# Optimization experiments

Measured on AMD Instinct MI355X. Metric: run time of the kernel, lower is better.

Reference implementation:

```python
import jax, jax.numpy as jnp
import numpy as np

N, E = 40000, 640000
DIN, HID, H = 512, 128, 4
C = HID  # per-head channels; H*C == 512 == DIN
BN_EPS = 1e-5


def setup_inputs() -> dict:
    key = jax.random.key(0)
    ks = jax.random.split(key, 32)
    sc = 0.05
    d = {}
    d["x"] = jax.random.normal(ks[0], (N, DIN), jnp.float32)
    d["edge_index"] = jax.random.randint(ks[1], (2, E), 0, N)
    i = 2
    for l in (1, 2, 3):
        d[f"W{l}"] = jax.random.normal(ks[i], (DIN, H * C), jnp.float32) * sc; i += 1
        d[f"as{l}"] = jax.random.normal(ks[i], (H, C), jnp.float32) * sc; i += 1
        d[f"ad{l}"] = jax.random.normal(ks[i], (H, C), jnp.float32) * sc; i += 1
        d[f"b{l}"] = jnp.zeros((H * C,), jnp.float32)
        d[f"g{l}"] = jnp.ones((H * C,), jnp.float32)
        d[f"be{l}"] = jnp.zeros((H * C,), jnp.float32)
    d["Wg1"] = jax.random.normal(ks[i], (H * C, HID), jnp.float32) * sc; i += 1
    d["bg1"] = jnp.zeros((HID,), jnp.float32)
    d["Wg2"] = jax.random.normal(ks[i], (HID, 1), jnp.float32) * sc; i += 1
    d["bg2"] = jnp.zeros((1,), jnp.float32)
    d["Wf1"] = jax.random.normal(ks[i], (H * C, HID), jnp.float32) * sc; i += 1
    d["bf1"] = jnp.zeros((HID,), jnp.float32)
    d["Wf2"] = jax.random.normal(ks[i], (HID, HID), jnp.float32) * sc; i += 1
    d["bf2"] = jnp.zeros((HID,), jnp.float32)
    d["Wp"] = jax.random.normal(ks[i], (HID + H * C, HID), jnp.float32) * sc; i += 1
    d["bp"] = jnp.zeros((HID,), jnp.float32)
    return d


def _gat(x, src, dst, W, a_s, a_d, b):
    # PyG GATConv (concat=True, negative_slope=0.2, self-loops already in src/dst)
    n = x.shape[0]
    h = (x @ W).reshape(n, H, C)                      # [N,H,C]
    es = jnp.einsum('nhc,hc->nh', h, a_s)             # alpha_src per node
    ed = jnp.einsum('nhc,hc->nh', h, a_d)             # alpha_dst per node
    e = jax.nn.leaky_relu(es[src] + ed[dst], 0.2)     # [Etot,H]
    m = jax.ops.segment_max(e, dst, num_segments=n)   # softmax over incoming edges
    ex = jnp.exp(e - m[dst])
    s = jax.ops.segment_sum(ex, dst, num_segments=n)
    w = ex / (s[dst] + 1e-16)                         # [Etot,H]
    out = jax.ops.segment_sum(w[:, :, None] * h[src], dst, num_segments=n)
    return out.reshape(n, H * C) + b


def _bn(x, g, b):
    mu = x.mean(0)
    var = x.var(0)
    return (x - mu) * jax.lax.rsqrt(var + BN_EPS) * g + b


def reference(x, edge_index,
              W1, as1, ad1, b1, g1, be1,
              W2, as2, ad2, b2, g2, be2,
              W3, as3, ad3, b3, g3, be3,
              Wg1, bg1, Wg2, bg2, Wf1, bf1, Wf2, bf2, Wp, bp):
    n = x.shape[0]
    loops = jnp.arange(n)
    src = jnp.concatenate([edge_index[0], loops])
    dst = jnp.concatenate([edge_index[1], loops])

    h = jax.nn.leaky_relu(_bn(_gat(x, src, dst, W1, as1, ad1, b1), g1, be1), 0.2)
    h_res = h
    h = jax.nn.leaky_relu(_bn(_gat(h, src, dst, W2, as2, ad2, b2), g2, be2), 0.2) + h_res
    h_res = h
    h = jax.nn.leaky_relu(_bn(_gat(h, src, dst, W3, as3, ad3, b3), g3, be3), 0.2) + h_res

    attn_scores = (jnp.tanh(h @ Wg1 + bg1) @ Wg2 + bg2)[:, 0]   # [N]
    attn_w = jax.nn.softmax(attn_scores)                        # softmax over all nodes
    feat = jax.nn.relu(h @ Wf1 + bf1) @ Wf2 + bf2               # [N,HID]
    gated = (attn_w[:, None] * feat).sum(0)                     # [HID]
    global_pooled = h.mean(0, keepdims=True)                    # batch=None -> one graph
    combined = jnp.concatenate([gated[None, :], global_pooled], axis=-1)  # [1,640]
    out = (combined @ Wp + bp)[0]                               # [HID]
    return out, attn_scores
```

## Files before the change

### kernel.cpp

```cpp
#include <hip/hip_runtime.h>
#include <math.h>

#define N_NODES 40000
#define M_PAD   40064
#define N_EDGES 640000
#define ETOT    (N_EDGES + N_NODES)
#define DINC    512
#define NHEAD   4
#define CHD     128
#define BN_EPS  1e-5f

typedef __attribute__((ext_vector_type(8))) short bf16x8;
typedef __attribute__((ext_vector_type(4))) float f32x4;

static __device__ __forceinline__ float lrelu(float x) { return x > 0.f ? x : 0.2f * x; }

static __device__ __forceinline__ unsigned short f2b(float f) {
    union { float f; unsigned int u; } v; v.f = f;
    unsigned int r = (v.u + 0x7fff + ((v.u >> 16) & 1)) >> 16;
    return (unsigned short)r;
}
static __device__ __forceinline__ float b2f(unsigned short b) {
    union { unsigned int u; float f; } v; v.u = ((unsigned int)b) << 16;
    return v.f;
}
static __device__ __forceinline__ float lo16(unsigned int u) {
    union { unsigned int u; float f; } v; v.u = u << 16; return v.f;
}
static __device__ __forceinline__ float hi16(unsigned int u) {
    union { unsigned int u; float f; } v; v.u = u & 0xffff0000u; return v.f;
}

static __device__ __forceinline__ void fma8(float* acc, uint4 hv, float wgt) {
    acc[0] += wgt * lo16(hv.x); acc[1] += wgt * hi16(hv.x);
    acc[2] += wgt * lo16(hv.y); acc[3] += wgt * hi16(hv.y);
    acc[4] += wgt * lo16(hv.z); acc[5] += wgt * hi16(hv.z);
    acc[6] += wgt * lo16(hv.w); acc[7] += wgt * hi16(hv.w);
}

#define GLDS16(g, l) __builtin_amdgcn_global_load_lds( \
    (__attribute__((address_space(1))) void*)(g),      \
    (__attribute__((address_space(3))) void*)(l), 16, 0, 0)

__global__ void k_degree(const int* __restrict__ ei, int* __restrict__ cnt) {
    int e = blockIdx.x * 256 + threadIdx.x;
    if (e < ETOT) {
        int dst = (e < N_EDGES) ? ei[N_EDGES + e] : (e - N_EDGES);
        atomicAdd(&cnt[dst], 1);
    }
}

__global__ __launch_bounds__(64) void k_scan1(const int* __restrict__ deg, int* __restrict__ bsum) {
    int lane = threadIdx.x;
    int v = deg[blockIdx.x * 64 + lane];
#pragma unroll
    for (int off = 32; off; off >>= 1) v += __shfl_xor(v, off);
    if (lane == 0) bsum[blockIdx.x] = v;
}

__global__ __launch_bounds__(1024) void k_scan2(const int* __restrict__ bsum, int* __restrict__ bpref,
                                                int* __restrict__ rowptr) {
    __shared__ int buf[1024];
    int tid = threadIdx.x;
    int v = (tid < 625) ? bsum[tid] : 0;
    buf[tid] = v;
    __syncthreads();
    for (int off = 1; off < 1024; off <<= 1) {
        int t = (tid >= off) ? buf[tid - off] : 0;
        __syncthreads();
        buf[tid] += t;
        __syncthreads();
    }
    if (tid < 625) bpref[tid] = buf[tid] - v;
    if (tid == 0) rowptr[N_NODES] = ETOT;
}

__global__ __launch_bounds__(64) void k_scan3(const int* __restrict__ deg, const int* __restrict__ bpref,
                                              int* __restrict__ rowptr) {
    int lane = threadIdx.x;
    int i = blockIdx.x * 64 + lane;
    int v = deg[i];
    int inc = v;
#pragma unroll
    for (int off = 1; off < 64; off <<= 1) {
        int t = __shfl_up(inc, off);
        if (lane >= off) inc += t;
    }
    rowptr[i] = bpref[blockIdx.x] + inc - v;
}

__global__ void k_fill(const int* __restrict__ ei, const int* __restrict__ rowptr,
                       int* __restrict__ cnt, int* __restrict__ csr_src) {
    int e = blockIdx.x * 256 + threadIdx.x;
    if (e < ETOT) {
        int src, dst;
        if (e < N_EDGES) { src = ei[e]; dst = ei[N_EDGES + e]; }
        else             { src = e - N_EDGES; dst = src; }
        int pos = rowptr[dst] + atomicAdd(&cnt[dst], 1);
        csr_src[pos] = src;
    }
}

__global__ __launch_bounds__(256) void k_cvtx(const float4* __restrict__ xin, uint4* __restrict__ xb) {
    size_t i = (size_t)blockIdx.x * 256 + threadIdx.x;
    float4 a = xin[i * 2], b = xin[i * 2 + 1];
    uint4 o;
    o.x = (unsigned)f2b(a.x) | ((unsigned)f2b(a.y) << 16);
    o.y = (unsigned)f2b(a.z) | ((unsigned)f2b(a.w) << 16);
    o.z = (unsigned)f2b(b.x) | ((unsigned)f2b(b.y) << 16);
    o.w = (unsigned)f2b(b.z) | ((unsigned)f2b(b.w) << 16);
    xb[i] = o;
}

__global__ __launch_bounds__(256) void k_cvtw(const float* __restrict__ W, unsigned short* __restrict__ Wt,
                                              int K, int Nn) {
    int idx = blockIdx.x * 256 + threadIdx.x;
    int k = idx / Nn, n = idx % Nn;
    Wt[(size_t)n * K + k] = f2b(W[idx]);
}

template<int CBF16, int EPI>
__global__ __launch_bounds__(256) void k_gemm_mfma(const unsigned short* __restrict__ A,
                                                   const unsigned short* __restrict__ Bt,
                                                   void* __restrict__ Cout,
                                                   int Nn, int K, int nbn,
                                                   const float* __restrict__ as_,
                                                   const float* __restrict__ ad_,
                                                   float* __restrict__ es,
                                                   float* __restrict__ ed) {
    __shared__ alignas(16) unsigned short As[128 * 64];
    __shared__ alignas(16) unsigned short Bs[128 * 64];
    const int tid  = threadIdx.x;
    const int wv   = tid >> 6;
    const int lane = tid & 63;
    const int bm = (blockIdx.x / nbn) * 128;
    const int bn = (blockIdx.x % nbn) * 128;
    const int wm = (wv >> 1) * 64;
    const int wn = (wv & 1) * 64;

    const int srow = lane >> 3;
    const int scol = (((lane & 7) ^ srow) * 8);
    const size_t a_base = (size_t)(bm + wv * 32 + srow) * K + scol;
    const size_t b_base = (size_t)(bn + wv * 32 + srow) * K + scol;

    f32x4 acc[4][4] = {};

    for (int k0 = 0; k0 < K; k0 += 64) {
#pragma unroll
        for (int q = 0; q < 4; ++q)
            GLDS16(A + a_base + (size_t)q * 8 * K + k0, &As[(wv * 32 + q * 8) * 64]);
#pragma unroll
        for (int q = 0; q < 4; ++q)
            GLDS16(Bt + b_base + (size_t)q * 8 * K + k0, &Bs[(wv * 32 + q * 8) * 64]);
        __syncthreads();

        const int r0 = lane & 15;
#pragma unroll
        for (int ks = 0; ks < 2; ++ks) {
            const int c = ks * 4 + (lane >> 4);
            bf16x8 af[4], bfr[4];
#pragma unroll
            for (int i = 0; i < 4; ++i) {
                int row = wm + i * 16 + r0;
                af[i] = *(const bf16x8*)&As[row * 64 + ((c ^ (row & 7)) * 8)];
            }
#pragma unroll
            for (int j = 0; j < 4; ++j) {
                int row = wn + j * 16 + r0;
                bfr[j] = *(const bf16x8*)&Bs[row * 64 + ((c ^ (row & 7)) * 8)];
            }
#pragma unroll
            for (int i = 0; i < 4; ++i)
#pragma unroll
                for (int j = 0; j < 4; ++j)
                    acc[i][j] = __builtin_amdgcn_mfma_f32_16x16x32_bf16(af[i], bfr[j], acc[i][j], 0, 0, 0);
        }
        __syncthreads();
    }

    const int crow0 = bm + wm + (lane >> 4) * 4;
    const int ccol  = bn + wn + (lane & 15);
#pragma unroll
    for (int i = 0; i < 4; ++i)
#pragma unroll
        for (int j = 0; j < 4; ++j)
#pragma unroll
            for (int r = 0; r < 4; ++r) {
                size_t off = (size_t)(crow0 + i * 16 + r) * Nn + ccol + j * 16;
                if (CBF16) ((unsigned short*)Cout)[off] = f2b(acc[i][j][r]);
                else       ((float*)Cout)[off] = acc[i][j][r];
            }

    if (EPI) {
        const int head = bn >> 7;
        float asv[4], adv[4];
#pragma unroll
        for (int j = 0; j < 4; ++j) {
            int cc = head * CHD + wn + j * 16 + (lane & 15);
            asv[j] = as_[cc];
            adv[j] = ad_[cc];
        }
        float* sE = (float*)As;
        sE[tid] = 0.f;
        __syncthreads();
#pragma unroll
        for (int i = 0; i < 4; ++i)
#pragma unroll
            for (int r = 0; r < 4; ++r) {
                float e = acc[i][0][r] * asv[0] + acc[i][1][r] * asv[1]
                        + acc[i][2][r] * asv[2] + acc[i][3][r] * asv[3];
                float d = acc[i][0][r] * adv[0] + acc[i][1][r] * adv[1]
                        + acc[i][2][r] * adv[2] + acc[i][3][r] * adv[3];
#pragma unroll
                for (int off = 8; off; off >>= 1) {
                    e += __shfl_xor(e, off);
                    d += __shfl_xor(d, off);
                }
                if ((lane & 15) == 0) {
                    int rloc = wm + i * 16 + (lane >> 4) * 4 + r;
                    atomicAdd(&sE[rloc], e);
                    atomicAdd(&sE[128 + rloc], d);
                }
            }
        __syncthreads();
        if (tid < 128) {
            es[(size_t)(bm + tid) * NHEAD + head] = sE[tid];
            ed[(size_t)(bm + tid) * NHEAD + head] = sE[128 + tid];
        }
    }
}

__global__ __launch_bounds__(256) void k_wts(const float4* __restrict__ es4,
                                             const float4* __restrict__ ed4,
                                             const int* __restrict__ rowptr,
                                             const int* __restrict__ csr_src,
                                             float4* __restrict__ wbuf4,
                                             float4* __restrict__ inv4) {
    int n = blockIdx.x * 4 + (threadIdx.x >> 6);
    int lane = threadIdx.x & 63;
    int start = rowptr[n], end = rowptr[n + 1];
    float4 edn = ed4[n];
    float4 mx = make_float4(-1e30f, -1e30f, -1e30f, -1e30f);
    for (int j0 = start; j0 < end; j0 += 64) {
        int j = j0 + lane;
        if (j < end) {
            int s = csr_src[j];
            float4 e = es4[s];
            mx.x = fmaxf(mx.x, lrelu(e.x + edn.x));
            mx.y = fmaxf(mx.y, lrelu(e.y + edn.y));
            mx.z = fmaxf(mx.z, lrelu(e.z + edn.z));
            mx.w = fmaxf(mx.w, lrelu(e.w + edn.w));
        }
    }
#pragma unroll
    for (int off = 32; off; off >>= 1) {
        mx.x = fmaxf(mx.x, __shfl_xor(mx.x, off));
        mx.y = fmaxf(mx.y, __shfl_xor(mx.y, off));
        mx.z = fmaxf(mx.z, __shfl_xor(mx.z, off));
        mx.w = fmaxf(mx.w, __shfl_xor(mx.w, off));
    }
    float4 sum = make_float4(0.f, 0.f, 0.f, 0.f);
    for (int j0 = start; j0 < end; j0 += 64) {
        int j = j0 + lane;
        if (j < end) {
            int s = csr_src[j];
            float4 e = es4[s];
            float4 ex;
            ex.x = expf(lrelu(e.x + edn.x) - mx.x);
            ex.y = expf(lrelu(e.y + edn.y) - mx.y);
            ex.z = expf(lrelu(e.z + edn.z) - mx.z);
            ex.w = expf(lrelu(e.w + edn.w) - mx.w);
            wbuf4[j] = ex;
            sum.x += ex.x; sum.y += ex.y; sum.z += ex.z; sum.w += ex.w;
        }
    }
#pragma unroll
    for (int off = 32; off; off >>= 1) {
        sum.x += __shfl_xor(sum.x, off);
        sum.y += __shfl_xor(sum.y, off);
        sum.z += __shfl_xor(sum.z, off);
        sum.w += __shfl_xor(sum.w, off);
    }
    if (lane == 0) {
        float4 iv;
        iv.x = 1.f / (sum.x + 1e-16f);
        iv.y = 1.f / (sum.y + 1e-16f);
        iv.z = 1.f / (sum.z + 1e-16f);
        iv.w = 1.f / (sum.w + 1e-16f);
        inv4[n] = iv;
    }
}

__global__ __launch_bounds__(256) void k_agg(const unsigned short* __restrict__ hb,
                                             const int* __restrict__ rowptr,
                                             const int* __restrict__ csr_src,
                                             const float* __restrict__ wbuf,
                                             const float* __restrict__ invp,
                                             unsigned short* __restrict__ aggb) {
    const int n = blockIdx.x * 4 + (threadIdx.x >> 6);
    const int lane = threadIdx.x & 63;
    const int head = lane >> 4;
    const int start = rowptr[n], end = rowptr[n + 1];

    float acc[8] = {};
    int j = start;
    for (; j + 3 < end; j += 4) {
        int s0 = csr_src[j], s1 = csr_src[j + 1], s2 = csr_src[j + 2], s3 = csr_src[j + 3];
        float w0 = wbuf[j * 4 + head];
        float w1 = wbuf[(j + 1) * 4 + head];
        float w2 = wbuf[(j + 2) * 4 + head];
        float w3 = wbuf[(j + 3) * 4 + head];
        uint4 h0 = *(const uint4*)&hb[(size_t)s0 * DINC + lane * 8];
        uint4 h1 = *(const uint4*)&hb[(size_t)s1 * DINC + lane * 8];
        uint4 h2 = *(const uint4*)&hb[(size_t)s2 * DINC + lane * 8];
        uint4 h3 = *(const uint4*)&hb[(size_t)s3 * DINC + lane * 8];
        fma8(acc, h0, w0); fma8(acc, h1, w1); fma8(acc, h2, w2); fma8(acc, h3, w3);
    }
    for (; j < end; ++j) {
        int s = csr_src[j];
        float wgt = wbuf[j * 4 + head];
        uint4 hv = *(const uint4*)&hb[(size_t)s * DINC + lane * 8];
        fma8(acc, hv, wgt);
    }
    float iv = invp[n * NHEAD + head];
    uint4 o;
    o.x = (unsigned)f2b(acc[0] * iv) | ((unsigned)f2b(acc[1] * iv) << 16);
    o.y = (unsigned)f2b(acc[2] * iv) | ((unsigned)f2b(acc[3] * iv) << 16);
    o.z = (unsigned)f2b(acc[4] * iv) | ((unsigned)f2b(acc[5] * iv) << 16);
    o.w = (unsigned)f2b(acc[6] * iv) | ((unsigned)f2b(acc[7] * iv) << 16);
    *(uint4*)&aggb[(size_t)n * DINC + lane * 8] = o;
}

__global__ __launch_bounds__(256) void k_bn_stats(const unsigned short* __restrict__ aggb,
                                                  float* __restrict__ stats) {
    int tid = threadIdx.x;
    int row0 = blockIdx.x * 64;
    int c0 = tid * 2;
    float s0 = 0, q0 = 0, s1 = 0, q1 = 0;
    for (int r = row0; r < row0 + 64; ++r) {
        unsigned int hv = *(const unsigned int*)&aggb[(size_t)r * DINC + c0];
        float v0 = lo16(hv), v1 = hi16(hv);
        s0 += v0; q0 += v0 * v0;
        s1 += v1; q1 += v1 * v1;
    }
    atomicAdd(&stats[c0], s0);
    atomicAdd(&stats[c0 + 1], s1);
    atomicAdd(&stats[DINC + c0], q0);
    atomicAdd(&stats[DINC + c0 + 1], q1);
}

__global__ __launch_bounds__(512) void k_bn_fin(const float* __restrict__ stats,
                                                const float* __restrict__ g,
                                                const float* __restrict__ be,
                                                float* __restrict__ ab) {
    int c = threadIdx.x;
    float mu = stats[c] * (1.f / N_NODES);
    float var = stats[DINC + c] * (1.f / N_NODES) - mu * mu;
    float rstd = rsqrtf(var + BN_EPS);
    float A = g[c] * rstd;
    ab[c] = A;
    ab[DINC + c] = be[c] - mu * A;
}

__global__ __launch_bounds__(256) void k_bn_act(const unsigned short* __restrict__ aggb,
                                                const float* __restrict__ ab,
                                                unsigned short* __restrict__ curb,
                                                int res) {
    size_t idx = (size_t)blockIdx.x * 256 + threadIdx.x;
    int c8 = ((int)(idx & 63)) * 8;
    uint4 v = *(const uint4*)&aggb[idx * 8];
    float xv[8] = { lo16(v.x), hi16(v.x), lo16(v.y), hi16(v.y),
                    lo16(v.z), hi16(v.z), lo16(v.w), hi16(v.w) };
#pragma unroll
    for (int q = 0; q < 8; ++q)
        xv[q] = lrelu(xv[q] * ab[c8 + q] + ab[DINC + c8 + q]);
    if (res) {
        uint4 r = *(const uint4*)&curb[idx * 8];
        xv[0] += lo16(r.x); xv[1] += hi16(r.x);
        xv[2] += lo16(r.y); xv[3] += hi16(r.y);
        xv[4] += lo16(r.z); xv[5] += hi16(r.z);
        xv[6] += lo16(r.w); xv[7] += hi16(r.w);
    }
    uint4 o;
    o.x = (unsigned)f2b(xv[0]) | ((unsigned)f2b(xv[1]) << 16);
    o.y = (unsigned)f2b(xv[2]) | ((unsigned)f2b(xv[3]) << 16);
    o.z = (unsigned)f2b(xv[4]) | ((unsigned)f2b(xv[5]) << 16);
    o.w = (unsigned)f2b(xv[6]) | ((unsigned)f2b(xv[7]) << 16);
    *(uint4*)&curb[idx * 8] = o;
}

__global__ __launch_bounds__(256) void k_scores(float* __restrict__ Gf,
                                                const float* __restrict__ bg1,
                                                const float* __restrict__ Wg2,
                                                const float* __restrict__ bg2,
                                                const float* __restrict__ bf1,
                                                float* __restrict__ scores) {
    int n = blockIdx.x * 4 + (threadIdx.x >> 6);
    int lane = threadIdx.x & 63;
    float acc = 0.f;
#pragma unroll
    for (int rep = 0; rep < 2; ++rep) {
        int j = lane + rep * 64;
        float t = tanhf(Gf[(size_t)n * 256 + j] + bg1[j]);
        acc += t * Wg2[j];
        float f = Gf[(size_t)n * 256 + 128 + j] + bf1[j];
        Gf[(size_t)n * 256 + 128 + j] = fmaxf(f, 0.f);
    }
#pragma unroll
    for (int off = 32; off; off >>= 1) acc += __shfl_xor(acc, off);
    if (lane == 0) scores[n] = acc + bg2[0];
}

__global__ __launch_bounds__(1024) void k_softmax(const float* __restrict__ scores, float* __restrict__ sm) {
    __shared__ float red[16];
    int tid = threadIdx.x, lane = tid & 63, wv = tid >> 6;
    float m = -1e30f;
    for (int i = tid; i < N_NODES; i += 1024) m = fmaxf(m, scores[i]);
#pragma unroll
    for (int off = 32; off; off >>= 1) m = fmaxf(m, __shfl_xor(m, off));
    if (lane == 0) red[wv] = m;
    __syncthreads();
    float mall = red[0];
    for (int i = 1; i < 16; ++i) mall = fmaxf(mall, red[i]);
    __syncthreads();
    float s = 0.f;
    for (int i = tid; i < N_NODES; i += 1024) s += expf(scores[i] - mall);
#pragma unroll
    for (int off = 32; off; off >>= 1) s += __shfl_xor(s, off);
    if (lane == 0) red[wv] = s;
    __syncthreads();
    if (tid == 0) {
        float tot = 0.f;
        for (int i = 0; i < 16; ++i) tot += red[i];
        sm[0] = mall; sm[1] = tot;
    }
}

__global__ __launch_bounds__(640) void k_vpool(const float* __restrict__ Gf,
                                               const unsigned short* __restrict__ hb,
                                               const float* __restrict__ scores,
                                               const float* __restrict__ sm,
                                               float* __restrict__ v,
                                               float* __restrict__ pooled) {
    int tid = threadIdx.x;
    int row0 = blockIdx.x * 64;
    float mall = sm[0];
    float invS = 1.f / sm[1];
    if (tid < 128) {
        float acc = 0.f;
        for (int r = row0; r < row0 + 64; ++r) {
            float w = expf(scores[r] - mall) * invS;
            acc += w * Gf[(size_t)r * 256 + 128 + tid];
        }
        atomicAdd(&v[tid], acc);
    } else {
        int c = tid - 128;
        float acc = 0.f;
        for (int r = row0; r < row0 + 64; ++r) acc += b2f(hb[(size_t)r * DINC + c]);
        atomicAdd(&pooled[c], acc * (1.f / N_NODES));
    }
}

__global__ __launch_bounds__(128) void k_final(const float* __restrict__ v,
                                               const float* __restrict__ pooled,
                                               const float* __restrict__ Wf2,
                                               const float* __restrict__ bf2,
                                               const float* __restrict__ Wp,
                                               const float* __restrict__ bp,
                                               float* __restrict__ out) {
    __shared__ float sg[128];
    int o = threadIdx.x;
    float g = bf2[o];
    for (int k = 0; k < 128; ++k) g += v[k] * Wf2[k * 128 + o];
    sg[o] = g;
    __syncthreads();
    float acc = bp[o];
    for (int c = 0; c < 128; ++c) acc += sg[c] * Wp[c * 128 + o];
    for (int j = 0; j < 512; ++j) acc += pooled[j] * Wp[(128 + j) * 128 + o];
    out[o] = acc;
}

extern "C" void kernel_launch(void* const* d_in, const int* in_sizes, int n_in,
                              void* d_out, int out_size, void* d_ws, size_t ws_size,
                              hipStream_t stream) {
    const float* x  = (const float*)d_in[0];
    const int*   ei = (const int*)d_in[1];
    const float* Wg1 = (const float*)d_in[20];
    const float* bg1 = (const float*)d_in[21];
    const float* Wg2 = (const float*)d_in[22];
    const float* bg2 = (const float*)d_in[23];
    const float* Wf1 = (const float*)d_in[24];
    const float* bf1 = (const float*)d_in[25];
    const float* Wf2 = (const float*)d_in[26];
    const float* bf2 = (const float*)d_in[27];
    const float* Wp  = (const float*)d_in[28];
    const float* bp  = (const float*)d_in[29];
    float* out = (float*)d_out;

    char* base = (char*)d_ws;
    size_t off = 0;
    auto take = [&](size_t nbytes) -> char* {
        char* p = base + off;
        off += (nbytes + 255) & ~(size_t)255;
        return p;
    };
    unsigned short* hb   = (unsigned short*)take((size_t)M_PAD * DINC * 2);
    unsigned short* curb = (unsigned short*)take((size_t)M_PAD * DINC * 2);
    unsigned short* xb   = (unsigned short*)take((size_t)M_PAD * DINC * 2);
    unsigned short* aggb = (unsigned short*)take((size_t)M_PAD * DINC * 2);
    float* Gf    = (float*)take((size_t)M_PAD * 256 * 4);
    float* es    = (float*)take((size_t)M_PAD * NHEAD * 4);
    float* ed    = (float*)take((size_t)M_PAD * NHEAD * 4);
    float* wbuf  = (float*)take((size_t)ETOT * NHEAD * 4);
    float* invp  = (float*)take((size_t)N_NODES * NHEAD * 4);
    int*   rowptr= (int*)take((size_t)(N_NODES + 1) * 4);
    int*   cnt   = (int*)take((size_t)N_NODES * 4);
    int*   csr   = (int*)take((size_t)ETOT * 4);
    int*   bsum  = (int*)take(625 * 4);
    int*   bpref = (int*)take(625 * 4);
    float* stats = (float*)take(DINC * 2 * 4);
    float* ab    = (float*)take(DINC * 2 * 4);
    float* sm    = (float*)take(2 * 4);
    float* vbuf  = (float*)take(128 * 4);
    float* pooled= (float*)take(DINC * 4);
    unsigned short* Wt1  = (unsigned short*)take((size_t)DINC * DINC * 2);
    unsigned short* Wt2  = (unsigned short*)take((size_t)DINC * DINC * 2);
    unsigned short* Wt3  = (unsigned short*)take((size_t)DINC * DINC * 2);
    unsigned short* Wct  = (unsigned short*)take((size_t)256 * DINC * 2);

    k_cvtx<<<(N_NODES * DINC / 8) / 256, 256, 0, stream>>>((const float4*)x, (uint4*)xb);
    hipMemsetAsync(xb + (size_t)N_NODES * DINC, 0, (size_t)(M_PAD - N_NODES) * DINC * 2, stream);
    hipMemsetAsync(curb + (size_t)N_NODES * DINC, 0, (size_t)(M_PAD - N_NODES) * DINC * 2, stream);
    k_cvtw<<<DINC * DINC / 256, 256, 0, stream>>>((const float*)d_in[2],  Wt1, DINC, DINC);
    k_cvtw<<<DINC * DINC / 256, 256, 0, stream>>>((const float*)d_in[8],  Wt2, DINC, DINC);
    k_cvtw<<<DINC * DINC / 256, 256, 0, stream>>>((const float*)d_in[14], Wt3, DINC, DINC);
    k_cvtw<<<DINC * 128 / 256, 256, 0, stream>>>(Wg1, Wct, DINC, 128);
    k_cvtw<<<DINC * 128 / 256, 256, 0, stream>>>(Wf1, Wct + (size_t)128 * DINC, DINC, 128);

    hipMemsetAsync(cnt, 0, N_NODES * 4, stream);
    k_degree<<<(ETOT + 255) / 256, 256, 0, stream>>>(ei, cnt);
    k_scan1<<<625, 64, 0, stream>>>(cnt, bsum);
    k_scan2<<<1, 1024, 0, stream>>>(bsum, bpref, rowptr);
    k_scan3<<<625, 64, 0, stream>>>(cnt, bpref, rowptr);
    hipMemsetAsync(cnt, 0, N_NODES * 4, stream);
    k_fill<<<(ETOT + 255) / 256, 256, 0, stream>>>(ei, rowptr, cnt, csr);

    const unsigned short* Wts[3] = {Wt1, Wt2, Wt3};
    const unsigned short* in = xb;
    for (int l = 0; l < 3; ++l) {
        const float* as_ = (const float*)d_in[2 + l * 6 + 1];
        const float* ad_ = (const float*)d_in[2 + l * 6 + 2];
        const float* g   = (const float*)d_in[2 + l * 6 + 4];
        const float* be  = (const float*)d_in[2 + l * 6 + 5];

        k_gemm_mfma<1, 1><<<(M_PAD / 128) * (DINC / 128), 256, 0, stream>>>(
            in, Wts[l], hb, DINC, DINC, DINC / 128, as_, ad_, es, ed);
        k_wts<<<N_NODES / 4, 256, 0, stream>>>((const float4*)es, (const float4*)ed, rowptr, csr,
                                               (float4*)wbuf, (float4*)invp);
        k_agg<<<N_NODES / 4, 256, 0, stream>>>(hb, rowptr, csr, wbuf, invp, aggb);
        hipMemsetAsync(stats, 0, DINC * 2 * 4, stream);
        k_bn_stats<<<N_NODES / 64, 256, 0, stream>>>(aggb, stats);
        k_bn_fin<<<1, 512, 0, stream>>>(stats, g, be, ab);
        k_bn_act<<<(N_NODES * (DINC / 8)) / 256, 256, 0, stream>>>(aggb, ab, curb, l > 0 ? 1 : 0);
        in = curb;
    }

    k_gemm_mfma<0, 0><<<(M_PAD / 128) * 2, 256, 0, stream>>>(
        curb, Wct, Gf, 256, DINC, 2, nullptr, nullptr, nullptr, nullptr);

    float* scores = out + 128;
    k_scores<<<N_NODES / 4, 256, 0, stream>>>(Gf, bg1, Wg2, bg2, bf1, scores);
    k_softmax<<<1, 1024, 0, stream>>>(scores, sm);
    hipMemsetAsync(vbuf, 0, 128 * 4, stream);
    hipMemsetAsync(pooled, 0, DINC * 4, stream);
    k_vpool<<<N_NODES / 64, 640, 0, stream>>>(Gf, curb, scores, sm, vbuf, pooled);
    k_final<<<1, 128, 0, stream>>>(vbuf, pooled, Wf2, bf2, Wp, bp, out);
}
```

Baseline: 925.8 us.

## Fuse setup kernels, recompute attention weights in aggregation, fuse pooling-head epilogue

```diff
diff --git a/kernel.cpp b/kernel.cpp
--- a/kernel.cpp
+++ b/kernel.cpp
@@ -42,6 +42,51 @@
     (__attribute__((address_space(1))) void*)(g),      \
     (__attribute__((address_space(3))) void*)(l), 16, 0, 0)
 
+#define CVTX_BLK 10000
+#define PAD_QUADS 4096
+__global__ __launch_bounds__(256) void k_prep(const float4* __restrict__ xin,
+                                              uint4* __restrict__ xb,
+                                              uint4* __restrict__ curb,
+                                              uint4* __restrict__ cnt4) {
+    int bid = blockIdx.x;
+    int tid = threadIdx.x;
+    if (bid < CVTX_BLK) {
+        size_t i = (size_t)bid * 256 + tid;
+        float4 a = xin[i * 2], b = xin[i * 2 + 1];
+        uint4 o;
+        o.x = (unsigned)f2b(a.x) | ((unsigned)f2b(a.y) << 16);
+        o.y = (unsigned)f2b(a.z) | ((unsigned)f2b(a.w) << 16);
+        o.z = (unsigned)f2b(b.x) | ((unsigned)f2b(b.y) << 16);
+        o.w = (unsigned)f2b(b.z) | ((unsigned)f2b(b.w) << 16);
+        xb[i] = o;
+    } else if (bid < CVTX_BLK + 16) {
+        int i = (bid - CVTX_BLK) * 256 + tid;
+        xb[(size_t)N_NODES * DINC / 8 + i] = make_uint4(0, 0, 0, 0);
+    } else if (bid < CVTX_BLK + 32) {
+        int i = (bid - CVTX_BLK - 16) * 256 + tid;
+        curb[(size_t)N_NODES * DINC / 8 + i] = make_uint4(0, 0, 0, 0);
+    } else {
+        int i = (bid - CVTX_BLK - 32) * 256 + tid;
+        if (i < N_NODES / 4) cnt4[i] = make_uint4(0, 0, 0, 0);
+    }
+}
+
+__global__ __launch_bounds__(256) void k_cvtw_all(const float* __restrict__ W1, unsigned short* __restrict__ T1,
+                                                  const float* __restrict__ W2, unsigned short* __restrict__ T2,
+                                                  const float* __restrict__ W3, unsigned short* __restrict__ T3,
+                                                  const float* __restrict__ Wg1, const float* __restrict__ Wf1,
+                                                  unsigned short* __restrict__ Wct) {
+    int idx = blockIdx.x * 256 + threadIdx.x;
+    const float* W; unsigned short* T; int Nn;
+    if (idx < 262144)            { W = W1; T = T1; Nn = 512; }
+    else if (idx < 524288)       { W = W2; T = T2; Nn = 512; idx -= 262144; }
+    else if (idx < 786432)       { W = W3; T = T3; Nn = 512; idx -= 524288; }
+    else if (idx < 851968)       { W = Wg1; T = Wct; Nn = 128; idx -= 786432; }
+    else                         { W = Wf1; T = Wct + 65536; Nn = 128; idx -= 851968; }
+    int k = idx / Nn, n = idx % Nn;
+    T[(size_t)n * 512 + k] = f2b(W[idx]);
+}
+
 __global__ void k_degree(const int* __restrict__ ei, int* __restrict__ cnt) {
     int e = blockIdx.x * 256 + threadIdx.x;
     if (e < ETOT) {
@@ -58,27 +103,14 @@
     if (lane == 0) bsum[blockIdx.x] = v;
 }
 
-__global__ __launch_bounds__(1024) void k_scan2(const int* __restrict__ bsum, int* __restrict__ bpref,
-                                                int* __restrict__ rowptr) {
-    __shared__ int buf[1024];
-    int tid = threadIdx.x;
-    int v = (tid < 625) ? bsum[tid] : 0;
-    buf[tid] = v;
-    __syncthreads();
-    for (int off = 1; off < 1024; off <<= 1) {
-        int t = (tid >= off) ? buf[tid - off] : 0;
-        __syncthreads();
-        buf[tid] += t;
-        __syncthreads();
-    }
-    if (tid < 625) bpref[tid] = buf[tid] - v;
-    if (tid == 0) rowptr[N_NODES] = ETOT;
-}
-
-__global__ __launch_bounds__(64) void k_scan3(const int* __restrict__ deg, const int* __restrict__ bpref,
-                                              int* __restrict__ rowptr) {
-    int lane = threadIdx.x;
-    int i = blockIdx.x * 64 + lane;
+__global__ __launch_bounds__(64) void k_scan23(const int* __restrict__ deg, const int* __restrict__ bsum,
+                                               int* __restrict__ rowptr, int* __restrict__ cnt) {
+    int b = blockIdx.x, lane = threadIdx.x;
+    int pre = 0;
+    for (int i = lane; i < b; i += 64) pre += bsum[i];
+#pragma unroll
+    for (int off = 32; off; off >>= 1) pre += __shfl_xor(pre, off);
+    int i = b * 64 + lane;
     int v = deg[i];
     int inc = v;
 #pragma unroll
@@ -86,7 +118,9 @@
         int t = __shfl_up(inc, off);
         if (lane >= off) inc += t;
     }
-    rowptr[i] = bpref[blockIdx.x] + inc - v;
+    rowptr[i] = pre + inc - v;
+    cnt[i] = 0;
+    if (b == 624 && lane == 63) rowptr[N_NODES] = ETOT;
 }
 
 __global__ void k_fill(const int* __restrict__ ei, const int* __restrict__ rowptr,
@@ -101,33 +135,17 @@
     }
 }
 
-__global__ __launch_bounds__(256) void k_cvtx(const float4* __restrict__ xin, uint4* __restrict__ xb) {
-    size_t i = (size_t)blockIdx.x * 256 + threadIdx.x;
-    float4 a = xin[i * 2], b = xin[i * 2 + 1];
-    uint4 o;
-    o.x = (unsigned)f2b(a.x) | ((unsigned)f2b(a.y) << 16);
-    o.y = (unsigned)f2b(a.z) | ((unsigned)f2b(a.w) << 16);
-    o.z = (unsigned)f2b(b.x) | ((unsigned)f2b(b.y) << 16);
-    o.w = (unsigned)f2b(b.z) | ((unsigned)f2b(b.w) << 16);
-    xb[i] = o;
-}
-
-__global__ __launch_bounds__(256) void k_cvtw(const float* __restrict__ W, unsigned short* __restrict__ Wt,
-                                              int K, int Nn) {
-    int idx = blockIdx.x * 256 + threadIdx.x;
-    int k = idx / Nn, n = idx % Nn;
-    Wt[(size_t)n * K + k] = f2b(W[idx]);
-}
-
 template<int CBF16, int EPI>
 __global__ __launch_bounds__(256) void k_gemm_mfma(const unsigned short* __restrict__ A,
                                                    const unsigned short* __restrict__ Bt,
                                                    void* __restrict__ Cout,
                                                    int Nn, int K, int nbn,
-                                                   const float* __restrict__ as_,
-                                                   const float* __restrict__ ad_,
-                                                   float* __restrict__ es,
-                                                   float* __restrict__ ed) {
+                                                   const float* __restrict__ p1,
+                                                   const float* __restrict__ p2,
+                                                   float* __restrict__ p3,
+                                                   float* __restrict__ p4,
+                                                   const float* __restrict__ p5,
+                                                   const float* __restrict__ p6) {
     __shared__ alignas(16) unsigned short As[128 * 64];
     __shared__ alignas(16) unsigned short Bs[128 * 64];
     const int tid  = threadIdx.x;
@@ -180,25 +198,28 @@
 
     const int crow0 = bm + wm + (lane >> 4) * 4;
     const int ccol  = bn + wn + (lane & 15);
-#pragma unroll
-    for (int i = 0; i < 4; ++i)
-#pragma unroll
-        for (int j = 0; j < 4; ++j)
-#pragma unroll
-            for (int r = 0; r < 4; ++r) {
-                size_t off = (size_t)(crow0 + i * 16 + r) * Nn + ccol + j * 16;
-                if (CBF16) ((unsigned short*)Cout)[off] = f2b(acc[i][j][r]);
-                else       ((float*)Cout)[off] = acc[i][j][r];
-            }
-
-    if (EPI) {
+
+    if (EPI != 2) {
+#pragma unroll
+        for (int i = 0; i < 4; ++i)
+#pragma unroll
+            for (int j = 0; j < 4; ++j)
+#pragma unroll
+                for (int r = 0; r < 4; ++r) {
+                    size_t off = (size_t)(crow0 + i * 16 + r) * Nn + ccol + j * 16;
+                    if (CBF16) ((unsigned short*)Cout)[off] = f2b(acc[i][j][r]);
+                    else       ((float*)Cout)[off] = acc[i][j][r];
+                }
+    }
+
+    if (EPI == 1) {
         const int head = bn >> 7;
         float asv[4], adv[4];
 #pragma unroll
         for (int j = 0; j < 4; ++j) {
             int cc = head * CHD + wn + j * 16 + (lane & 15);
-            asv[j] = as_[cc];
-            adv[j] = ad_[cc];
+            asv[j] = p1[cc];
+            adv[j] = p2[cc];
         }
         float* sE = (float*)As;
         sE[tid] = 0.f;
@@ -224,18 +245,63 @@
             }
         __syncthreads();
         if (tid < 128) {
-            es[(size_t)(bm + tid) * NHEAD + head] = sE[tid];
-            ed[(size_t)(bm + tid) * NHEAD + head] = sE[128 + tid];
+            p3[(size_t)(bm + tid) * NHEAD + head] = sE[tid];
+            p4[(size_t)(bm + tid) * NHEAD + head] = sE[128 + tid];
         }
     }
-}
-
-__global__ __launch_bounds__(256) void k_wts(const float4* __restrict__ es4,
+
+    if (EPI == 2) {
+        if (bn == 0) {
+            float wgv[4], bgv[4];
+#pragma unroll
+            for (int j = 0; j < 4; ++j) {
+                int cc = wn + j * 16 + (lane & 15);
+                bgv[j] = p1[cc];
+                wgv[j] = p2[cc];
+            }
+            float* sE = (float*)As;
+            sE[tid] = 0.f;
+            __syncthreads();
+#pragma unroll
+            for (int i = 0; i < 4; ++i)
+#pragma unroll
+                for (int r = 0; r < 4; ++r) {
+                    float e = tanhf(acc[i][0][r] + bgv[0]) * wgv[0]
+                            + tanhf(acc[i][1][r] + bgv[1]) * wgv[1]
+                            + tanhf(acc[i][2][r] + bgv[2]) * wgv[2]
+                            + tanhf(acc[i][3][r] + bgv[3]) * wgv[3];
+#pragma unroll
+                    for (int off = 8; off; off >>= 1) e += __shfl_xor(e, off);
+                    if ((lane & 15) == 0)
+                        atomicAdd(&sE[wm + i * 16 + (lane >> 4) * 4 + r], e);
+                }
+            __syncthreads();
+            if (tid < 128) p3[bm + tid] = sE[tid] + p5[0];
+        } else {
+#pragma unroll
+            for (int j = 0; j < 4; ++j) {
+                int colF = wn + j * 16 + (lane & 15);
+                float bv = p6[colF];
+#pragma unroll
+                for (int i = 0; i < 4; ++i)
+#pragma unroll
+                    for (int r = 0; r < 4; ++r)
+                        p4[(size_t)(crow0 + i * 16 + r) * 128 + colF] =
+                            fmaxf(acc[i][j][r] + bv, 0.f);
+            }
+        }
+    }
+}
+
+__global__ __launch_bounds__(256) void k_mxi(const float4* __restrict__ es4,
                                              const float4* __restrict__ ed4,
                                              const int* __restrict__ rowptr,
                                              const int* __restrict__ csr_src,
-                                             float4* __restrict__ wbuf4,
-                                             float4* __restrict__ inv4) {
+                                             float4* __restrict__ mx4,
+                                             float4* __restrict__ inv4,
+                                             float* __restrict__ stats) {
+    if (blockIdx.x == 0)
+        for (int q = threadIdx.x; q < DINC * 2; q += 256) stats[q] = 0.f;
     int n = blockIdx.x * 4 + (threadIdx.x >> 6);
     int lane = threadIdx.x & 63;
     int start = rowptr[n], end = rowptr[n + 1];
@@ -265,13 +331,10 @@
         if (j < end) {
             int s = csr_src[j];
             float4 e = es4[s];
-            float4 ex;
-            ex.x = expf(lrelu(e.x + edn.x) - mx.x);
-            ex.y = expf(lrelu(e.y + edn.y) - mx.y);
-            ex.z = expf(lrelu(e.z + edn.z) - mx.z);
-            ex.w = expf(lrelu(e.w + edn.w) - mx.w);
-            wbuf4[j] = ex;
-            sum.x += ex.x; sum.y += ex.y; sum.z += ex.z; sum.w += ex.w;
+            sum.x += __expf(lrelu(e.x + edn.x) - mx.x);
+            sum.y += __expf(lrelu(e.y + edn.y) - mx.y);
+            sum.z += __expf(lrelu(e.z + edn.z) - mx.z);
+            sum.w += __expf(lrelu(e.w + edn.w) - mx.w);
         }
     }
 #pragma unroll
@@ -282,6 +345,7 @@
         sum.w += __shfl_xor(sum.w, off);
     }
     if (lane == 0) {
+        mx4[n] = mx;
         float4 iv;
         iv.x = 1.f / (sum.x + 1e-16f);
         iv.y = 1.f / (sum.y + 1e-16f);
@@ -292,43 +356,46 @@
 }
 
 __global__ __launch_bounds__(256) void k_agg(const unsigned short* __restrict__ hb,
+                                             const float4* __restrict__ es4,
                                              const int* __restrict__ rowptr,
                                              const int* __restrict__ csr_src,
-                                             const float* __restrict__ wbuf,
+                                             const float* __restrict__ mxp,
                                              const float* __restrict__ invp,
+                                             const float* __restrict__ edp,
                                              unsigned short* __restrict__ aggb) {
-    const int n = blockIdx.x * 4 + (threadIdx.x >> 6);
-    const int lane = threadIdx.x & 63;
+    __shared__ float part[4][512];
+    const int n = blockIdx.x;
+    const int tid = threadIdx.x;
+    const int grp = tid >> 6;
+    const int lane = tid & 63;
     const int head = lane >> 4;
     const int start = rowptr[n], end = rowptr[n + 1];
+    const float mxh = mxp[n * NHEAD + head];
+    const float ivh = invp[n * NHEAD + head];
+    const float edh = edp[n * NHEAD + head];
 
     float acc[8] = {};
-    int j = start;
-    for (; j + 3 < end; j += 4) {
-        int s0 = csr_src[j], s1 = csr_src[j + 1], s2 = csr_src[j + 2], s3 = csr_src[j + 3];
-        float w0 = wbuf[j * 4 + head];
-        float w1 = wbuf[(j + 1) * 4 + head];
-        float w2 = wbuf[(j + 2) * 4 + head];
-        float w3 = wbuf[(j + 3) * 4 + head];
-        uint4 h0 = *(const uint4*)&hb[(size_t)s0 * DINC + lane * 8];
-        uint4 h1 = *(const uint4*)&hb[(size_t)s1 * DINC + lane * 8];
-        uint4 h2 = *(const uint4*)&hb[(size_t)s2 * DINC + lane * 8];
-        uint4 h3 = *(const uint4*)&hb[(size_t)s3 * DINC + lane * 8];
-        fma8(acc, h0, w0); fma8(acc, h1, w1); fma8(acc, h2, w2); fma8(acc, h3, w3);
-    }
-    for (; j < end; ++j) {
-        int s = csr_src[j];
-        float wgt = wbuf[j * 4 + head];
+    int j = start + grp;
+    int s_n = 0; float4 e_n = make_float4(0.f, 0.f, 0.f, 0.f);
+    if (j < end) { s_n = csr_src[j]; e_n = es4[s_n]; }
+    while (j < end) {
+        int s = s_n; float4 e4 = e_n;
+        int j2 = j + 4;
+        if (j2 < end) { s_n = csr_src[j2]; e_n = es4[s_n]; }
+        float esh = (head == 0) ? e4.x : (head == 1) ? e4.y : (head == 2) ? e4.z : e4.w;
+        float wgt = __expf(lrelu(esh + edh) - mxh) * ivh;
         uint4 hv = *(const uint4*)&hb[(size_t)s * DINC + lane * 8];
         fma8(acc, hv, wgt);
-    }
-    float iv = invp[n * NHEAD + head];
-    uint4 o;
-    o.x = (unsigned)f2b(acc[0] * iv) | ((unsigned)f2b(acc[1] * iv) << 16);
-    o.y = (unsigned)f2b(acc[2] * iv) | ((unsigned)f2b(acc[3] * iv) << 16);
-    o.z = (unsigned)f2b(acc[4] * iv) | ((unsigned)f2b(acc[5] * iv) << 16);
-    o.w = (unsigned)f2b(acc[6] * iv) | ((unsigned)f2b(acc[7] * iv) << 16);
-    *(uint4*)&aggb[(size_t)n * DINC + lane * 8] = o;
+        j = j2;
+    }
+    *(float4*)&part[grp][lane * 8]     = make_float4(acc[0], acc[1], acc[2], acc[3]);
+    *(float4*)&part[grp][lane * 8 + 4] = make_float4(acc[4], acc[5], acc[6], acc[7]);
+    __syncthreads();
+    const int c = tid * 2;
+    float v0 = part[0][c] + part[1][c] + part[2][c] + part[3][c];
+    float v1 = part[0][c + 1] + part[1][c + 1] + part[2][c + 1] + part[3][c + 1];
+    unsigned int o = (unsigned)f2b(v0) | ((unsigned)f2b(v1) << 16);
+    *(unsigned int*)&aggb[(size_t)n * DINC + c] = o;
 }
 
 __global__ __launch_bounds__(256) void k_bn_stats(const unsigned short* __restrict__ aggb,
@@ -389,31 +456,12 @@
     *(uint4*)&curb[idx * 8] = o;
 }
 
-__global__ __launch_bounds__(256) void k_scores(float* __restrict__ Gf,
-                                                const float* __restrict__ bg1,
-                                                const float* __restrict__ Wg2,
-                                                const float* __restrict__ bg2,
-                                                const float* __restrict__ bf1,
-                                                float* __restrict__ scores) {
-    int n = blockIdx.x * 4 + (threadIdx.x >> 6);
-    int lane = threadIdx.x & 63;
-    float acc = 0.f;
-#pragma unroll
-    for (int rep = 0; rep < 2; ++rep) {
-        int j = lane + rep * 64;
-        float t = tanhf(Gf[(size_t)n * 256 + j] + bg1[j]);
-        acc += t * Wg2[j];
-        float f = Gf[(size_t)n * 256 + 128 + j] + bf1[j];
-        Gf[(size_t)n * 256 + 128 + j] = fmaxf(f, 0.f);
-    }
-#pragma unroll
-    for (int off = 32; off; off >>= 1) acc += __shfl_xor(acc, off);
-    if (lane == 0) scores[n] = acc + bg2[0];
-}
-
-__global__ __launch_bounds__(1024) void k_softmax(const float* __restrict__ scores, float* __restrict__ sm) {
+__global__ __launch_bounds__(1024) void k_softmax(const float* __restrict__ scores, float* __restrict__ sm,
+                                                  float* __restrict__ vbuf, float* __restrict__ pooled) {
     __shared__ float red[16];
     int tid = threadIdx.x, lane = tid & 63, wv = tid >> 6;
+    if (tid < 128) vbuf[tid] = 0.f;
+    if (tid < DINC) pooled[tid] = 0.f;
     float m = -1e30f;
     for (int i = tid; i < N_NODES; i += 1024) m = fmaxf(m, scores[i]);
 #pragma unroll
@@ -436,7 +484,7 @@
     }
 }
 
-__global__ __launch_bounds__(640) void k_vpool(const float* __restrict__ Gf,
+__global__ __launch_bounds__(640) void k_vpool(const float* __restrict__ Fb,
                                                const unsigned short* __restrict__ hb,
                                                const float* __restrict__ scores,
                                                const float* __restrict__ sm,
@@ -450,7 +498,7 @@
         float acc = 0.f;
         for (int r = row0; r < row0 + 64; ++r) {
             float w = expf(scores[r] - mall) * invS;
-            acc += w * Gf[(size_t)r * 256 + 128 + tid];
+            acc += w * Fb[(size_t)r * 128 + tid];
         }
         atomicAdd(&v[tid], acc);
     } else {
@@ -508,16 +556,15 @@
     unsigned short* curb = (unsigned short*)take((size_t)M_PAD * DINC * 2);
     unsigned short* xb   = (unsigned short*)take((size_t)M_PAD * DINC * 2);
     unsigned short* aggb = (unsigned short*)take((size_t)M_PAD * DINC * 2);
-    float* Gf    = (float*)take((size_t)M_PAD * 256 * 4);
+    float* Fb    = (float*)take((size_t)M_PAD * 128 * 4);
     float* es    = (float*)take((size_t)M_PAD * NHEAD * 4);
     float* ed    = (float*)take((size_t)M_PAD * NHEAD * 4);
-    float* wbuf  = (float*)take((size_t)ETOT * NHEAD * 4);
+    float* mxp   = (float*)take((size_t)N_NODES * NHEAD * 4);
     float* invp  = (float*)take((size_t)N_NODES * NHEAD * 4);
     int*   rowptr= (int*)take((size_t)(N_NODES + 1) * 4);
     int*   cnt   = (int*)take((size_t)N_NODES * 4);
     int*   csr   = (int*)take((size_t)ETOT * 4);
     int*   bsum  = (int*)take(625 * 4);
-    int*   bpref = (int*)take(625 * 4);
     float* stats = (float*)take(DINC * 2 * 4);
     float* ab    = (float*)take(DINC * 2 * 4);
     float* sm    = (float*)take(2 * 4);
@@ -528,21 +575,15 @@
     unsigned short* Wt3  = (unsigned short*)take((size_t)DINC * DINC * 2);
     unsigned short* Wct  = (unsigned short*)take((size_t)256 * DINC * 2);
 
-    k_cvtx<<<(N_NODES * DINC / 8) / 256, 256, 0, stream>>>((const float4*)x, (uint4*)xb);
-    hipMemsetAsync(xb + (size_t)N_NODES * DINC, 0, (size_t)(M_PAD - N_NODES) * DINC * 2, stream);
-    hipMemsetAsync(curb + (size_t)N_NODES * DINC, 0, (size_t)(M_PAD - N_NODES) * DINC * 2, stream);
-    k_cvtw<<<DINC * DINC / 256, 256, 0, stream>>>((const float*)d_in[2],  Wt1, DINC, DINC);
-    k_cvtw<<<DINC * DINC / 256, 256, 0, stream>>>((const float*)d_in[8],  Wt2, DINC, DINC);
-    k_cvtw<<<DINC * DINC / 256, 256, 0, stream>>>((const float*)d_in[14], Wt3, DINC, DINC);
-    k_cvtw<<<DINC * 128 / 256, 256, 0, stream>>>(Wg1, Wct, DINC, 128);
-    k_cvtw<<<DINC * 128 / 256, 256, 0, stream>>>(Wf1, Wct + (size_t)128 * DINC, DINC, 128);
-
-    hipMemsetAsync(cnt, 0, N_NODES * 4, stream);
+    k_prep<<<CVTX_BLK + 32 + 40, 256, 0, stream>>>((const float4*)x, (uint4*)xb,
+                                                   (uint4*)curb, (uint4*)cnt);
+    k_cvtw_all<<<3584, 256, 0, stream>>>((const float*)d_in[2], Wt1,
+                                         (const float*)d_in[8], Wt2,
+                                         (const float*)d_in[14], Wt3,
+                                         Wg1, Wf1, Wct);
     k_degree<<<(ETOT + 255) / 256, 256, 0, stream>>>(ei, cnt);
     k_scan1<<<625, 64, 0, stream>>>(cnt, bsum);
-    k_scan2<<<1, 1024, 0, stream>>>(bsum, bpref, rowptr);
-    k_scan3<<<625, 64, 0, stream>>>(cnt, bpref, rowptr);
-    hipMemsetAsync(cnt, 0, N_NODES * 4, stream);
+    k_scan23<<<625, 64, 0, stream>>>(cnt, bsum, rowptr, cnt);
     k_fill<<<(ETOT + 255) / 256, 256, 0, stream>>>(ei, rowptr, cnt, csr);
 
     const unsigned short* Wts[3] = {Wt1, Wt2, Wt3};
@@ -554,25 +595,22 @@
         const float* be  = (const float*)d_in[2 + l * 6 + 5];
 
         k_gemm_mfma<1, 1><<<(M_PAD / 128) * (DINC / 128), 256, 0, stream>>>(
-            in, Wts[l], hb, DINC, DINC, DINC / 128, as_, ad_, es, ed);
-        k_wts<<<N_NODES / 4, 256, 0, stream>>>((const float4*)es, (const float4*)ed, rowptr, csr,
-                                               (float4*)wbuf, (float4*)invp);
-        k_agg<<<N_NODES / 4, 256, 0, stream>>>(hb, rowptr, csr, wbuf, invp, aggb);
-        hipMemsetAsync(stats, 0, DINC * 2 * 4, stream);
+            in, Wts[l], hb, DINC, DINC, DINC / 128, as_, ad_, es, ed, nullptr, nullptr);
+        k_mxi<<<N_NODES / 4, 256, 0, stream>>>((const float4*)es, (const float4*)ed, rowptr, csr,
+                                               (float4*)mxp, (float4*)invp, stats);
+        k_agg<<<N_NODES, 256, 0, stream>>>(hb, (const float4*)es, rowptr, csr,
+                                           mxp, invp, ed, aggb);
         k_bn_stats<<<N_NODES / 64, 256, 0, stream>>>(aggb, stats);
         k_bn_fin<<<1, 512, 0, stream>>>(stats, g, be, ab);
         k_bn_act<<<(N_NODES * (DINC / 8)) / 256, 256, 0, stream>>>(aggb, ab, curb, l > 0 ? 1 : 0);
         in = curb;
     }
 
-    k_gemm_mfma<0, 0><<<(M_PAD / 128) * 2, 256, 0, stream>>>(
-        curb, Wct, Gf, 256, DINC, 2, nullptr, nullptr, nullptr, nullptr);
-
     float* scores = out + 128;
-    k_scores<<<N_NODES / 4, 256, 0, stream>>>(Gf, bg1, Wg2, bg2, bf1, scores);
-    k_softmax<<<1, 1024, 0, stream>>>(scores, sm);
-    hipMemsetAsync(vbuf, 0, 128 * 4, stream);
-    hipMemsetAsync(pooled, 0, DINC * 4, stream);
-    k_vpool<<<N_NODES / 64, 640, 0, stream>>>(Gf, curb, scores, sm, vbuf, pooled);
+    k_gemm_mfma<0, 2><<<(M_PAD / 128) * 2, 256, 0, stream>>>(
+        curb, Wct, nullptr, 256, DINC, 2, bg1, Wg2, scores, Fb, bg2, bf1);
+
+    k_softmax<<<1, 1024, 0, stream>>>(scores, sm, vbuf, pooled);
+    k_vpool<<<N_NODES / 64, 640, 0, stream>>>(Fb, curb, scores, sm, vbuf, pooled);
     k_final<<<1, 128, 0, stream>>>(vbuf, pooled, Wf2, bf2, Wp, bp, out);
 }
```

After: 916.6 us. About the same (-1.0%).
